# Kernel tuning notes

Measured on AMD Instinct MI355X. Metric: run time of the kernel, lower is better.

Reference implementation:

```python
import jax, jax.numpy as jnp
import numpy as np

D = 1024      # input_size == embed_size == head_dim (heads=1, see shape constraints)
L = 1000      # seq len, capped by positional_encoding(1000, ...)
N = 16        # batch
HEADS = 1
NEG = -1e20


def _pos_encoding(position, d_model):
    # Faithful to source: get_angles with i = arange(0, d_model, 2) gives d_model//2 columns.
    pos = np.arange(position)[:, None].astype(np.float32)
    i = np.arange(0, d_model, 2)[None, :].astype(np.float32)
    angle_rates = 1.0 / np.power(10000.0, 2.0 * np.floor(i / 2.0) / np.float32(d_model))
    ang = pos * angle_rates  # [position, d_model//2]
    ang[:, 0::2] = np.sin(ang[:, 0::2])
    ang[:, 1::2] = np.cos(ang[:, 1::2])
    return jnp.asarray(ang[None], dtype=jnp.float32)  # [1, position, d_model//2]


def setup_inputs() -> dict:
    key = jax.random.key(0)
    ks = jax.random.split(key, 10)
    s = 1.0 / np.sqrt(D)
    return {
        "inputs": jax.random.normal(ks[0], (N, L, D), jnp.float32),
        "inputs2": jax.random.normal(ks[1], (N, L, D), jnp.float32),
        "Wq": jax.random.normal(ks[2], (D, D), jnp.float32) * s,
        "Wqu": jax.random.normal(ks[3], (D, D), jnp.float32) * s,
        "Wk": jax.random.normal(ks[4], (D, D), jnp.float32) * s,
        "Wv": jax.random.normal(ks[5], (D, D), jnp.float32) * s,
        "W_d": jax.random.normal(ks[6], (D, 2 * D), jnp.float32) * s,
        "h_vec": jax.random.normal(ks[7], (D, 1), jnp.float32) * s,
        "fc_w": jax.random.normal(ks[8], (D, D), jnp.float32) * s,
        "fc_b": jnp.zeros((D,), jnp.float32),
        "ln_g": jnp.ones((D,), jnp.float32),
        "ln_b": jnp.zeros((D,), jnp.float32),
    }


def reference(inputs, inputs2, Wq, Wqu, Wk, Wv, W_d, h_vec, fc_w, fc_b, ln_g, ln_b):
    pe = _pos_encoding(1000, 2 * D)[:, :L, :]  # [1, L, D]
    q = inputs + pe
    k = inputs + pe
    v = inputs + pe
    qu = inputs2 + pe

    # heads == 1: the per-head loop collapses to a single pass; energy /= heads is /1.
    qh = q @ Wq.T     # [N, L, D]
    kh = k @ Wk.T
    vh = v @ Wv.T
    quh = qu @ Wqu.T

    scale = 1.0 / HEADS
    e1 = jnp.einsum('nqd,nkd->nqk', qh, kh) * scale  # [N, L, L]
    e2 = jnp.einsum('nqd,nkd->nqk', quh, kh) * scale

    mask = jnp.tril(jnp.ones((L, L), jnp.float32))  # causal tril mask (mask=None path)
    e1 = jnp.where(mask == 0, NEG, e1)
    e2 = jnp.where(mask == 0, NEG, e2)

    a1 = jax.nn.softmax(e1, axis=-1)
    a2 = jax.nn.softmax(e2, axis=-1)

    out1 = jnp.einsum('nqk,nkd->nqd', a1, vh)  # [N, L, D]
    out2 = jnp.einsum('nqk,nkd->nqd', a2, vh)

    concat1 = jnp.concatenate([out1, inputs], axis=2)  # [N, L, 2D]
    hidden = jax.nn.relu(concat1 @ W_d.T)              # [N, L, D]
    E_c = hidden @ h_vec                               # [N, L, 1]
    E_u = hidden @ h_vec  # source bug: E_u also computed from concat1 (== E_c)
    A = jax.nn.sigmoid(E_c - E_u)  # == exp(Ec)/(exp(Ec)+exp(Eu)), stable form

    out = A * out1 + (1.0 - A) * out2  # [N, L, D]
    out = out + inputs

    mu = jnp.mean(out, axis=-1, keepdims=True)
    var = jnp.var(out, axis=-1, keepdims=True)
    out = (out - mu) / jnp.sqrt(var + 1e-5) * ln_g + ln_b

    return out @ fc_w.T + fc_b
```

## Files before the change

kernel.cpp:

```cpp
#include <hip/hip_runtime.h>
#include <stdint.h>


typedef unsigned short u16;
typedef unsigned long long u64;
typedef __attribute__((ext_vector_type(8))) short short8;
typedef __attribute__((ext_vector_type(4))) float f32x4;

__device__ __forceinline__ u16 bf16_rne(float f) {
  unsigned u = __float_as_uint(f);
  u = (u + 0x7FFFu + ((u >> 16) & 1u)) >> 16;
  return (u16)u;
}
__device__ __forceinline__ float bf16_f(u16 h) { return __uint_as_float(((unsigned)h) << 16); }

__device__ __forceinline__ void gload16(const u16* g, u16* l) {
  __builtin_amdgcn_global_load_lds(
      (const __attribute__((address_space(1))) void*)g,
      (__attribute__((address_space(3))) void*)l, 16, 0, 0);
}

__device__ __forceinline__ float wred_max(float v) {
#pragma unroll
  for (int o = 32; o > 0; o >>= 1) v = fmaxf(v, __shfl_xor(v, o));
  return v;
}
__device__ __forceinline__ float wred_sum(float v) {
#pragma unroll
  for (int o = 32; o > 0; o >>= 1) v += __shfl_xor(v, o);
  return v;
}

__global__ void sentinel_kernel(float* __restrict__ out, int n, float val) {
  for (int i = blockIdx.x * 256 + threadIdx.x; i < n; i += gridDim.x * 256) out[i] = val;
}

__global__ void pe_kernel(float* __restrict__ pe) {
  const int g = blockIdx.x * 256 + threadIdx.x;
  const int l = g >> 10, j = g & 1023;
  const float rate = powf(10000.0f, -(float)j * (1.0f / 1024.0f));
  const float ang = (float)l * rate;
  pe[g] = (j & 1) ? cosf(ang) : sinf(ang);
}

__global__ void splitx_kernel(const float* __restrict__ in, const float* __restrict__ pe,
                              u16* __restrict__ xh, u16* __restrict__ xl) {
  const size_t g = ((size_t)blockIdx.x * 256 + threadIdx.x) * 4;
  const int m = (int)(g >> 10), d = (int)(g & 1023);
  const int n = m >> 10, r = m & 1023;
  float a[4] = {0.f, 0.f, 0.f, 0.f};
  if (r < 1000) {
    const size_t src = (((size_t)n * 1000 + r) << 10) + d;
    const float4 v1 = *(const float4*)(in + src);
    const float4 p = *(const float4*)(pe + (((size_t)r) << 10) + d);
    a[0] = v1.x + p.x; a[1] = v1.y + p.y; a[2] = v1.z + p.z; a[3] = v1.w + p.w;
  }
  ushort4 oh, ol;
  u16 h;
  h = bf16_rne(a[0]); oh.x = h; ol.x = bf16_rne(a[0] - bf16_f(h));
  h = bf16_rne(a[1]); oh.y = h; ol.y = bf16_rne(a[1] - bf16_f(h));
  h = bf16_rne(a[2]); oh.z = h; ol.z = bf16_rne(a[2] - bf16_f(h));
  h = bf16_rne(a[3]); oh.w = h; ol.w = bf16_rne(a[3] - bf16_f(h));
  *(ushort4*)(xh + g) = oh;
  *(ushort4*)(xl + g) = ol;
}

__global__ void splitwT_kernel(const float* __restrict__ src, u16* __restrict__ hi,
                               u16* __restrict__ lo) {
  const int g = blockIdx.x * 256 + threadIdx.x;
  const int i = g >> 10, d = g & 1023;
  const float v = src[((size_t)d << 10) + i];
  const u16 h = bf16_rne(v);
  hi[g] = h;
  lo[g] = bf16_rne(v - bf16_f(h));
}

__global__ void splitw_plain(const float* __restrict__ src, u16* __restrict__ dst) {
  const size_t g = ((size_t)blockIdx.x * 256 + threadIdx.x) * 4;
  const float4 v = *(const float4*)(src + g);
  ushort4 o;
  o.x = bf16_rne(v.x); o.y = bf16_rne(v.y); o.z = bf16_rne(v.z); o.w = bf16_rne(v.w);
  *(ushort4*)(dst + g) = o;
}

__global__ void softmax_kernel(float* __restrict__ e) {
  const int q = blockIdx.x, nb = blockIdx.y, tid = threadIdx.x;
  const int qt = q >> 7, ql = q & 127, W = (qt + 1) << 7, len = q + 1;
  float* er = e + (size_t)nb * 589824 + (size_t)16384 * (qt * (qt + 1) / 2) + (size_t)ql * W;
  const int k0 = tid * 4;
  const bool act = k0 < W;
  __shared__ float red[4];
  float v[4] = {0.f, 0.f, 0.f, 0.f};
  if (act) {
    const float4 ev = *(const float4*)(er + k0);
    v[0] = ev.x; v[1] = ev.y; v[2] = ev.z; v[3] = ev.w;
  }
  float m = -3.0e38f;
#pragma unroll
  for (int i = 0; i < 4; ++i)
    if (k0 + i < len) m = fmaxf(m, v[i]);
  m = wred_max(m);
  if ((tid & 63) == 0) red[tid >> 6] = m;
  __syncthreads();
  m = fmaxf(fmaxf(red[0], red[1]), fmaxf(red[2], red[3]));
  __syncthreads();
  float p[4];
  float s = 0.f;
#pragma unroll
  for (int i = 0; i < 4; ++i) {
    p[i] = (k0 + i < len) ? expf(v[i] - m) : 0.f;
    s += p[i];
  }
  s = wred_sum(s);
  if ((tid & 63) == 0) red[tid >> 6] = s;
  __syncthreads();
  s = red[0] + red[1] + red[2] + red[3];
  const float inv = 1.0f / s;
  if (act) {
    ushort4 o;
    o.x = bf16_rne(p[0] * inv); o.y = bf16_rne(p[1] * inv);
    o.z = bf16_rne(p[2] * inv); o.w = bf16_rne(p[3] * inv);
    *(ushort4*)((u16*)er + k0) = o;
  }
}

__global__ void ln_kernel(const u16* __restrict__ op, const float* __restrict__ inp,
                          const float* __restrict__ gam, const float* __restrict__ bet,
                          u16* __restrict__ yln) {
  const int r = blockIdx.x, n = blockIdx.y, tid = threadIdx.x;
  const size_t prow = (((((size_t)n) << 10) + r) << 10);
  const size_t crow = ((((size_t)n * 1000) + r) << 10);
  const int d0 = tid * 4;
  const ushort4 ov = *(const ushort4*)(op + prow + d0);
  const float4 x = *(const float4*)(inp + crow + d0);
  float y[4] = {bf16_f(ov.x) + x.x, bf16_f(ov.y) + x.y, bf16_f(ov.z) + x.z, bf16_f(ov.w) + x.w};
  float s = 0.f, ss = 0.f;
#pragma unroll
  for (int i = 0; i < 4; ++i) { s += y[i]; ss += y[i] * y[i]; }
  __shared__ float red[8];
  s = wred_sum(s);
  ss = wred_sum(ss);
  if ((tid & 63) == 0) { red[tid >> 6] = s; red[4 + (tid >> 6)] = ss; }
  __syncthreads();
  s = red[0] + red[1] + red[2] + red[3];
  ss = red[4] + red[5] + red[6] + red[7];
  const float mu = s * 0.0009765625f;
  const float var = ss * 0.0009765625f - mu * mu;
  const float rstd = rsqrtf(var + 1e-5f);
  const float4 gv = *(const float4*)(gam + d0);
  const float4 bv = *(const float4*)(bet + d0);
  ushort4 o;
  o.x = bf16_rne((y[0] - mu) * rstd * gv.x + bv.x);
  o.y = bf16_rne((y[1] - mu) * rstd * gv.y + bv.y);
  o.z = bf16_rne((y[2] - mu) * rstd * gv.z + bv.z);
  o.w = bf16_rne((y[3] - mu) * rstd * gv.w + bv.w);
  *(ushort4*)(yln + prow + d0) = o;
}

enum { G_SPLIT = 0, G_TRIL = 1, G_PV1 = 2, G_PV2 = 3, G_OUT = 4, G_FC = 5 };

template <int MODE>
__global__ __launch_bounds__(256, 2) void gemm_k(
    const u16* __restrict__ Ah, const u16* __restrict__ Al,
    const u16* __restrict__ Bh, const u16* __restrict__ Bl,
    void* C0, const float* __restrict__ bias) {
  constexpr bool SPLIT = (MODE == G_SPLIT || MODE == G_TRIL);
  constexpr bool PV = (MODE == G_PV1 || MODE == G_PV2);
  constexpr int NP = SPLIT ? 4 : 2;
  constexpr int BHB = SPLIT ? 32768 : 16384;

  __shared__ __align__(16) u16 smem[NP * 8192];

  const int tid = threadIdx.x, lane = tid & 63, w = tid >> 6;
  const int l8 = lane >> 3, jlo = lane & 7, jj = jlo ^ l8;
  const int wr = w >> 1, wc = w & 1;

  int qt = 0, kt = 0, nb = 0, mt = 0, nt = 0;
  int ksteps = 16, lda = 1024;

  size_t abase = 0, bbase = 0;
  if constexpr (MODE == G_SPLIT || MODE == G_OUT || MODE == G_FC) {
    mt = blockIdx.x >> 3; nt = blockIdx.x & 7;
    abase = ((size_t)mt * 128) << 10;
    bbase = ((size_t)nt * 128) << 10;
  } else if constexpr (MODE == G_TRIL) {
    qt = blockIdx.x; kt = blockIdx.y; nb = blockIdx.z;
    if (kt > qt) return;
    abase = (((size_t)(nb << 10)) + qt * 128) << 10;
    bbase = (((size_t)(nb << 10)) + kt * 128) << 10;
  } else {
    qt = blockIdx.x; kt = blockIdx.y; nb = blockIdx.z;
    const int W = (qt + 1) << 7;
    lda = 2 * W;
    ksteps = (qt + 1) * 2;
    abase = (size_t)nb * 1179648 + (size_t)32768 * (qt * (qt + 1) / 2);
  }

  const u16* gsA = Ah + abase + (size_t)(w * 8 + l8) * lda + jj * 8;
  const u16* gsAl = nullptr;
  const u16* gsB = nullptr;
  const u16* gsBl = nullptr;
  if constexpr (SPLIT) {
    gsAl = Al + abase + ((size_t)(w * 8 + l8) << 10) + jj * 8;
    gsB = Bh + bbase + ((size_t)(w * 8 + l8) << 10) + jj * 8;
    gsBl = Bl + bbase + ((size_t)(w * 8 + l8) << 10) + jj * 8;
  } else if constexpr (!PV) {
    gsB = Bh + bbase + ((size_t)(w * 8 + l8) << 10) + jj * 8;
  }

  const int slot = ((lane >> 4) ^ (lane & 7)) << 4;
  int aoff[4], boff[4];
#pragma unroll
  for (int f = 0; f < 4; ++f) {
    aoff[f] = (wr * 64 + f * 16 + (lane & 15)) * 128 + slot;
    boff[f] = (wc * 64 + f * 16 + (lane & 15)) * 128 + slot;
  }

  f32x4 acc[4][4];
#pragma unroll
  for (int i = 0; i < 4; ++i)
#pragma unroll
    for (int j = 0; j < 4; ++j)
#pragma unroll
      for (int q = 0; q < 4; ++q) acc[i][j][q] = 0.0f;

  for (int ks = 0; ks < ksteps; ++ks) {
#pragma unroll
    for (int i = 0; i < 4; ++i)
      gload16(gsA + (size_t)(i * 32) * lda, &smem[(i * 4 + w) * 512]);
    gsA += 64;
    if constexpr (SPLIT) {
#pragma unroll
      for (int i = 0; i < 4; ++i) {
        gload16(gsAl + ((size_t)(i * 32) << 10), &smem[8192 + (i * 4 + w) * 512]);
        gload16(gsB + ((size_t)(i * 32) << 10), &smem[16384 + (i * 4 + w) * 512]);
        gload16(gsBl + ((size_t)(i * 32) << 10), &smem[24576 + (i * 4 + w) * 512]);
      }
      gsAl += 64; gsB += 64; gsBl += 64;
    } else if constexpr (!PV) {
#pragma unroll
      for (int i = 0; i < 4; ++i)
        gload16(gsB + ((size_t)(i * 32) << 10), &smem[8192 + (i * 4 + w) * 512]);
      gsB += 64;
    } else {
      const int k4 = tid & 15, dch = tid >> 4;
      const u16* xs = Bh + (((size_t)(nb << 10) + ks * 64 + k4 * 4) << 10) + kt * 128 + dch * 8;
      uint4 q0 = *(const uint4*)xs;
      uint4 q1 = *(const uint4*)(xs + 1024);
      uint4 q2 = *(const uint4*)(xs + 2048);
      uint4 q3 = *(const uint4*)(xs + 3072);
      const u16* p0 = (const u16*)&q0;
      const u16* p1 = (const u16*)&q1;
      const u16* p2 = (const u16*)&q2;
      const u16* p3 = (const u16*)&q3;
#pragma unroll
      for (int dd = 0; dd < 8; ++dd) {
        const int row = dch * 8 + dd;
        const int sl = (k4 >> 1) ^ (row & 7);
        u64 pk = (u64)p0[dd] | ((u64)p1[dd] << 16) | ((u64)p2[dd] << 32) | ((u64)p3[dd] << 48);
        *(u64*)&smem[8192 + row * 64 + sl * 8 + (k4 & 1) * 4] = pk;
      }
    }
    __syncthreads();

    const char* sm = (const char*)smem;
#pragma unroll
    for (int half = 0; half < 2; ++half) {
      const int kx = half * 64;
      short8 fa[4], fb[4], fal[4], fbl[4];
#pragma unroll
      for (int f = 0; f < 4; ++f) {
        fa[f] = *(const short8*)(sm + (aoff[f] ^ kx));
        fb[f] = *(const short8*)(sm + BHB + (boff[f] ^ kx));
        if constexpr (SPLIT) {
          fal[f] = *(const short8*)(sm + 16384 + (aoff[f] ^ kx));
          fbl[f] = *(const short8*)(sm + BHB + 16384 + (boff[f] ^ kx));
        }
      }
#pragma unroll
      for (int fm = 0; fm < 4; ++fm)
#pragma unroll
        for (int fn = 0; fn < 4; ++fn) {
          acc[fm][fn] = __builtin_amdgcn_mfma_f32_16x16x32_bf16(fa[fm], fb[fn], acc[fm][fn], 0, 0, 0);
          if constexpr (SPLIT) {
            acc[fm][fn] = __builtin_amdgcn_mfma_f32_16x16x32_bf16(fa[fm], fbl[fn], acc[fm][fn], 0, 0, 0);
            acc[fm][fn] = __builtin_amdgcn_mfma_f32_16x16x32_bf16(fal[fm], fb[fn], acc[fm][fn], 0, 0, 0);
          }
        }
    }
    __syncthreads();
  }

#pragma unroll
  for (int fm = 0; fm < 4; ++fm) {
#pragma unroll
    for (int jr = 0; jr < 4; ++jr) {
      const int rr = wr * 64 + fm * 16 + ((lane >> 4) << 2) + jr;
#pragma unroll
      for (int fn = 0; fn < 4; ++fn) {
        const int ccl = wc * 64 + fn * 16 + (lane & 15);
        const float v = acc[fm][fn][jr];
        if constexpr (MODE == G_SPLIT) {
          const size_t idx = (((size_t)mt * 128 + rr) << 10) + nt * 128 + ccl;
          u16* hi = (u16*)C0;
          u16* lo = hi + (size_t)16 * 1024 * 1024;
          const u16 h = bf16_rne(v);
          hi[idx] = h;
          lo[idx] = bf16_rne(v - bf16_f(h));
        } else if constexpr (MODE == G_TRIL) {
          const size_t TBf = (size_t)nb * 589824 + (size_t)16384 * (qt * (qt + 1) / 2);
          ((float*)C0)[TBf + (size_t)rr * ((qt + 1) << 7) + kt * 128 + ccl] = v;
        } else if constexpr (MODE == G_PV1) {
          const size_t idx = (((size_t)(nb << 10) + qt * 128 + rr) << 10) + kt * 128 + ccl;
          ((u16*)C0)[idx] = bf16_rne(v);
        } else if constexpr (MODE == G_PV2) {
          const size_t idx = (((size_t)(nb << 10) + qt * 128 + rr) << 10) + kt * 128 + ccl;
          const float u1 = bf16_f(((u16*)C0)[idx]);
          ((u16*)C0)[idx] = bf16_rne(0.5f * (v + u1));
        } else if constexpr (MODE == G_OUT) {
          const size_t idx = (((size_t)mt * 128 + rr) << 10) + nt * 128 + ccl;
          ((u16*)C0)[idx] = bf16_rne(v);
        } else {
          const size_t R = (size_t)mt * 128 + rr;
          const size_t r2 = R & 1023, nn = R >> 10;
          if (r2 < 1000)
            ((float*)C0)[((nn * 1000 + r2) << 10) + nt * 128 + ccl] = v + bias[nt * 128 + ccl];
        }
      }
    }
  }
}

extern "C" void kernel_launch(void* const* d_in, const int* in_sizes, int n_in,
                              void* d_out, int out_size, void* d_ws, size_t ws_size,
                              hipStream_t stream) {
  (void)in_sizes; (void)n_in;
  const float* inputs  = (const float*)d_in[0];
  const float* inputs2 = (const float*)d_in[1];
  const float* Wq  = (const float*)d_in[2];
  const float* Wqu = (const float*)d_in[3];
  const float* Wk  = (const float*)d_in[4];
  const float* Wv  = (const float*)d_in[5];
  const float* fc_w = (const float*)d_in[8];
  const float* fc_b = (const float*)d_in[9];
  const float* ln_g = (const float*)d_in[10];
  const float* ln_b = (const float*)d_in[11];

  constexpr size_t MB = 1024ull * 1024ull;
  constexpr size_t NEED = 240ull * MB;
  if (ws_size < NEED) {
    sentinel_kernel<<<2048, 256, 0, stream>>>((float*)d_out, out_size,
                                              -1.0e6f - 1000.0f * (float)(ws_size >> 20));
    return;
  }

  char* ws = (char*)d_ws;
  u16* Wv_b   = (u16*)(ws + 0 * MB);
  u16* fcw_b  = (u16*)(ws + 2 * MB);
  u16* ST_h   = (u16*)(ws + 4 * MB);
  u16* SuT_h  = (u16*)(ws + 8 * MB);
  u16* x_h    = (u16*)(ws + 12 * MB);
  u16* xu_h   = (u16*)(ws + 76 * MB);
  u16* quS_h  = (u16*)(ws + 140 * MB);
  u16* WqT_h  = (u16*)(ws + 204 * MB);
  u16* WkT_h  = (u16*)(ws + 208 * MB);
  u16* WquT_h = (u16*)(ws + 212 * MB);
  float* pe   = (float*)(ws + 216 * MB);
  float* T    = (float*)(ws + 204 * MB);
  u16* U      = (u16*)(ws + 76 * MB);
  u16* outp   = (u16*)(ws + 108 * MB);
  u16* yln    = (u16*)(ws + 204 * MB);

  u16* ST_l  = (u16*)(ws + 6 * MB);
  u16* SuT_l = (u16*)(ws + 10 * MB);
  u16* x_l   = (u16*)(ws + 44 * MB);
  u16* xu_l  = (u16*)(ws + 108 * MB);
  u16* qS_h  = (u16*)(ws + 76 * MB);
  u16* qS_l  = (u16*)(ws + 108 * MB);
  u16* quS_l = (u16*)(ws + 172 * MB);
  u16* WqT_l  = (u16*)(ws + 206 * MB);
  u16* WkT_l  = (u16*)(ws + 210 * MB);
  u16* WquT_l = (u16*)(ws + 214 * MB);

  pe_kernel<<<4000, 256, 0, stream>>>(pe);
  splitwT_kernel<<<4096, 256, 0, stream>>>(Wq, WqT_h, WqT_l);
  splitwT_kernel<<<4096, 256, 0, stream>>>(Wk, WkT_h, WkT_l);
  splitwT_kernel<<<4096, 256, 0, stream>>>(Wqu, WquT_h, WquT_l);
  splitw_plain<<<1024, 256, 0, stream>>>(Wv, Wv_b);
  splitw_plain<<<1024, 256, 0, stream>>>(fc_w, fcw_b);
  gemm_k<G_SPLIT><<<64, 256, 0, stream>>>(WkT_h, WkT_l, WqT_h, WqT_l, ST_h, nullptr);
  gemm_k<G_SPLIT><<<64, 256, 0, stream>>>(WkT_h, WkT_l, WquT_h, WquT_l, SuT_h, nullptr);
  hipMemcpyAsync(ST_l, (u16*)(ws + 36 * MB), 2 * MB, hipMemcpyDeviceToDevice, stream);
  hipMemcpyAsync(SuT_l, (u16*)(ws + 40 * MB), 2 * MB, hipMemcpyDeviceToDevice, stream);
  splitx_kernel<<<16384, 256, 0, stream>>>(inputs, pe, x_h, x_l);
  splitx_kernel<<<16384, 256, 0, stream>>>(inputs2, pe, xu_h, xu_l);
  gemm_k<G_SPLIT><<<1024, 256, 0, stream>>>(xu_h, xu_l, SuT_h, SuT_l, quS_h, nullptr);
  gemm_k<G_SPLIT><<<1024, 256, 0, stream>>>(x_h, x_l, ST_h, ST_l, qS_h, nullptr);
  gemm_k<G_TRIL><<<dim3(8, 8, 16), 256, 0, stream>>>(qS_h, qS_l, x_h, x_l, T, nullptr);
  softmax_kernel<<<dim3(1024, 16), 256, 0, stream>>>(T);
  gemm_k<G_PV1><<<dim3(8, 8, 16), 256, 0, stream>>>((const u16*)T, nullptr, x_h, nullptr, U, nullptr);
  gemm_k<G_TRIL><<<dim3(8, 8, 16), 256, 0, stream>>>(quS_h, quS_l, x_h, x_l, T, nullptr);
  softmax_kernel<<<dim3(1024, 16), 256, 0, stream>>>(T);
  gemm_k<G_PV2><<<dim3(8, 8, 16), 256, 0, stream>>>((const u16*)T, nullptr, x_h, nullptr, U, nullptr);
  gemm_k<G_OUT><<<1024, 256, 0, stream>>>(U, nullptr, Wv_b, nullptr, outp, nullptr);
  ln_kernel<<<dim3(1000, 16), 256, 0, stream>>>(outp, inputs, ln_g, ln_b, yln);
  gemm_k<G_FC><<<1024, 256, 0, stream>>>(yln, nullptr, fcw_b, nullptr, (float*)d_out, fc_b);
}
```

Baseline: 946.9 us.

## Sum both attention matrices before a single PV GEMM and reorder grids

Since A is always 0.5, the output is 0.5*(P1+P2)@V. The second softmax now adds the stored first probabilities, so only one PV GEMM runs instead of two, and the read-modify-write of U is dropped. Separate T buffers are used and the workspace layout is reassigned. The change also swizzles block order for the dense GEMMs, puts batch first in the triangular grids, and raises the launch-bounds occupancy hint for the non-split GEMMs. Summing in bf16 before the matmul changes rounding slightly.

```diff
diff --git a/kernel.cpp b/kernel.cpp
--- a/kernel.cpp
+++ b/kernel.cpp
@@ -83,10 +83,12 @@
   *(ushort4*)(dst + g) = o;
 }
 
-__global__ void softmax_kernel(float* __restrict__ e) {
+template <bool ADD>
+__global__ void softmax_kernel(float* __restrict__ e, const u16* __restrict__ Pprev) {
   const int q = blockIdx.x, nb = blockIdx.y, tid = threadIdx.x;
   const int qt = q >> 7, ql = q & 127, W = (qt + 1) << 7, len = q + 1;
-  float* er = e + (size_t)nb * 589824 + (size_t)16384 * (qt * (qt + 1) / 2) + (size_t)ql * W;
+  const size_t rowoff = (size_t)nb * 589824 + (size_t)16384 * (qt * (qt + 1) / 2) + (size_t)ql * W;
+  float* er = e + rowoff;
   const int k0 = tid * 4;
   const bool act = k0 < W;
   __shared__ float red[4];
@@ -117,9 +119,14 @@
   s = red[0] + red[1] + red[2] + red[3];
   const float inv = 1.0f / s;
   if (act) {
+    float a1[4] = {0.f, 0.f, 0.f, 0.f};
+    if constexpr (ADD) {
+      const ushort4 pv = *(const ushort4*)(Pprev + 2 * rowoff + k0);
+      a1[0] = bf16_f(pv.x); a1[1] = bf16_f(pv.y); a1[2] = bf16_f(pv.z); a1[3] = bf16_f(pv.w);
+    }
     ushort4 o;
-    o.x = bf16_rne(p[0] * inv); o.y = bf16_rne(p[1] * inv);
-    o.z = bf16_rne(p[2] * inv); o.w = bf16_rne(p[3] * inv);
+    o.x = bf16_rne(p[0] * inv + a1[0]); o.y = bf16_rne(p[1] * inv + a1[1]);
+    o.z = bf16_rne(p[2] * inv + a1[2]); o.w = bf16_rne(p[3] * inv + a1[3]);
     *(ushort4*)((u16*)er + k0) = o;
   }
 }
@@ -157,15 +164,15 @@
   *(ushort4*)(yln + prow + d0) = o;
 }
 
-enum { G_SPLIT = 0, G_TRIL = 1, G_PV1 = 2, G_PV2 = 3, G_OUT = 4, G_FC = 5 };
+enum { G_SPLIT = 0, G_TRIL = 1, G_PV = 2, G_OUT = 3, G_FC = 4 };
 
 template <int MODE>
-__global__ __launch_bounds__(256, 2) void gemm_k(
-    const u16* __restrict__ Ah, const u16* __restrict__ Al,
-    const u16* __restrict__ Bh, const u16* __restrict__ Bl,
-    void* C0, const float* __restrict__ bias) {
+__global__ __launch_bounds__(256, (MODE == G_SPLIT || MODE == G_TRIL) ? 2 : 4)
+void gemm_k(const u16* __restrict__ Ah, const u16* __restrict__ Al,
+            const u16* __restrict__ Bh, const u16* __restrict__ Bl,
+            void* C0, const float* __restrict__ bias) {
   constexpr bool SPLIT = (MODE == G_SPLIT || MODE == G_TRIL);
-  constexpr bool PV = (MODE == G_PV1 || MODE == G_PV2);
+  constexpr bool PV = (MODE == G_PV);
   constexpr int NP = SPLIT ? 4 : 2;
   constexpr int BHB = SPLIT ? 32768 : 16384;
 
@@ -180,16 +187,18 @@
 
   size_t abase = 0, bbase = 0;
   if constexpr (MODE == G_SPLIT || MODE == G_OUT || MODE == G_FC) {
-    mt = blockIdx.x >> 3; nt = blockIdx.x & 7;
+    const int bid = blockIdx.x, n8 = gridDim.x >> 3;
+    const int nid = (bid & 7) * n8 + (bid >> 3);
+    mt = nid >> 3; nt = nid & 7;
     abase = ((size_t)mt * 128) << 10;
     bbase = ((size_t)nt * 128) << 10;
   } else if constexpr (MODE == G_TRIL) {
-    qt = blockIdx.x; kt = blockIdx.y; nb = blockIdx.z;
+    nb = blockIdx.x; qt = blockIdx.y; kt = blockIdx.z;
     if (kt > qt) return;
     abase = (((size_t)(nb << 10)) + qt * 128) << 10;
     bbase = (((size_t)(nb << 10)) + kt * 128) << 10;
   } else {
-    qt = blockIdx.x; kt = blockIdx.y; nb = blockIdx.z;
+    nb = blockIdx.x; qt = blockIdx.y; kt = blockIdx.z;
     const int W = (qt + 1) << 7;
     lda = 2 * W;
     ksteps = (qt + 1) * 2;
@@ -310,13 +319,9 @@
         } else if constexpr (MODE == G_TRIL) {
           const size_t TBf = (size_t)nb * 589824 + (size_t)16384 * (qt * (qt + 1) / 2);
           ((float*)C0)[TBf + (size_t)rr * ((qt + 1) << 7) + kt * 128 + ccl] = v;
-        } else if constexpr (MODE == G_PV1) {
+        } else if constexpr (MODE == G_PV) {
           const size_t idx = (((size_t)(nb << 10) + qt * 128 + rr) << 10) + kt * 128 + ccl;
-          ((u16*)C0)[idx] = bf16_rne(v);
-        } else if constexpr (MODE == G_PV2) {
-          const size_t idx = (((size_t)(nb << 10) + qt * 128 + rr) << 10) + kt * 128 + ccl;
-          const float u1 = bf16_f(((u16*)C0)[idx]);
-          ((u16*)C0)[idx] = bf16_rne(0.5f * (v + u1));
+          ((u16*)C0)[idx] = bf16_rne(0.5f * v);
         } else if constexpr (MODE == G_OUT) {
           const size_t idx = (((size_t)mt * 128 + rr) << 10) + nt * 128 + ccl;
           ((u16*)C0)[idx] = bf16_rne(v);
@@ -366,9 +371,10 @@
   u16* WkT_h  = (u16*)(ws + 208 * MB);
   u16* WquT_h = (u16*)(ws + 212 * MB);
   float* pe   = (float*)(ws + 216 * MB);
-  float* T    = (float*)(ws + 204 * MB);
-  u16* U      = (u16*)(ws + 76 * MB);
-  u16* outp   = (u16*)(ws + 108 * MB);
+  float* T1   = (float*)(ws + 204 * MB);
+  float* T2   = (float*)(ws + 76 * MB);
+  u16* U      = (u16*)(ws + 140 * MB);
+  u16* outp   = (u16*)(ws + 172 * MB);
   u16* yln    = (u16*)(ws + 204 * MB);
 
   u16* ST_l  = (u16*)(ws + 6 * MB);
@@ -396,12 +402,11 @@
   splitx_kernel<<<16384, 256, 0, stream>>>(inputs2, pe, xu_h, xu_l);
   gemm_k<G_SPLIT><<<1024, 256, 0, stream>>>(xu_h, xu_l, SuT_h, SuT_l, quS_h, nullptr);
   gemm_k<G_SPLIT><<<1024, 256, 0, stream>>>(x_h, x_l, ST_h, ST_l, qS_h, nullptr);
-  gemm_k<G_TRIL><<<dim3(8, 8, 16), 256, 0, stream>>>(qS_h, qS_l, x_h, x_l, T, nullptr);
-  softmax_kernel<<<dim3(1024, 16), 256, 0, stream>>>(T);
-  gemm_k<G_PV1><<<dim3(8, 8, 16), 256, 0, stream>>>((const u16*)T, nullptr, x_h, nullptr, U, nullptr);
-  gemm_k<G_TRIL><<<dim3(8, 8, 16), 256, 0, stream>>>(quS_h, quS_l, x_h, x_l, T, nullptr);
-  softmax_kernel<<<dim3(1024, 16), 256, 0, stream>>>(T);
-  gemm_k<G_PV2><<<dim3(8, 8, 16), 256, 0, stream>>>((const u16*)T, nullptr, x_h, nullptr, U, nullptr);
+  gemm_k<G_TRIL><<<dim3(16, 8, 8), 256, 0, stream>>>(qS_h, qS_l, x_h, x_l, T1, nullptr);
+  softmax_kernel<false><<<dim3(1024, 16), 256, 0, stream>>>(T1, nullptr);
+  gemm_k<G_TRIL><<<dim3(16, 8, 8), 256, 0, stream>>>(quS_h, quS_l, x_h, x_l, T2, nullptr);
+  softmax_kernel<true><<<dim3(1024, 16), 256, 0, stream>>>(T2, (const u16*)T1);
+  gemm_k<G_PV><<<dim3(16, 8, 8), 256, 0, stream>>>((const u16*)T2, nullptr, x_h, nullptr, U, nullptr);
   gemm_k<G_OUT><<<1024, 256, 0, stream>>>(U, nullptr, Wv_b, nullptr, outp, nullptr);
   ln_kernel<<<dim3(1000, 16), 256, 0, stream>>>(outp, inputs, ln_g, ln_b, yln);
   gemm_k<G_FC><<<1024, 256, 0, stream>>>(yln, nullptr, fcw_b, nullptr, (float*)d_out, fc_b);
```

New measurement: 818.2 us. -13.6%, faster.
